# Kernel tuning notes

Measured on AMD Instinct MI355X. Metric: run time of the kernel, lower is better.

The kernel has to match this reference:

```python
import jax, jax.numpy as jnp
import numpy as np

I = 4  # input size
H = 4  # hidden size


def setup_inputs() -> dict:
    key = jax.random.key(0)
    ks = jax.random.split(key, 7)
    T, B = 2048, 8192
    s = 1.0 / np.sqrt(H)  # torch LSTM/Linear init scale
    x = jax.random.normal(ks[0], (T, B, I), dtype=jnp.float32)
    w_ih = jax.random.uniform(ks[1], (4 * H, I), minval=-s, maxval=s, dtype=jnp.float32)
    w_hh = jax.random.uniform(ks[2], (4 * H, H), minval=-s, maxval=s, dtype=jnp.float32)
    b_ih = jax.random.uniform(ks[3], (4 * H,), minval=-s, maxval=s, dtype=jnp.float32)
    b_hh = jax.random.uniform(ks[4], (4 * H,), minval=-s, maxval=s, dtype=jnp.float32)
    w_lin = jax.random.uniform(ks[5], (1, H), minval=-0.5, maxval=0.5, dtype=jnp.float32)
    b_lin = jax.random.uniform(ks[6], (1,), minval=-0.5, maxval=0.5, dtype=jnp.float32)
    return {"x": x, "w_ih": w_ih, "w_hh": w_hh, "b_ih": b_ih, "b_hh": b_hh,
            "w_lin": w_lin, "b_lin": b_lin}


def _lstm_scan(x, w_ih, w_hh, b_ih, b_hh):
    # x: (T, B, I). PyTorch gate order: i, f, g, o.
    T, B, _ = x.shape
    b = b_ih + b_hh  # (4H,)
    # Precompute input projections for all timesteps: (T, B, 4H)
    xg = jnp.einsum('tbi,gi->tbg', x, w_ih) + b

    def step(carry, xg_t):
        h, c = carry  # (B, H) each
        gates = xg_t + h @ w_hh.T  # (B, 4H)
        i, f, g, o = jnp.split(gates, 4, axis=-1)
        i = jax.nn.sigmoid(i)
        f = jax.nn.sigmoid(f)
        g = jnp.tanh(g)
        o = jax.nn.sigmoid(o)
        c = f * c + i * g
        h = o * jnp.tanh(c)
        return (h, c), h

    h0 = jnp.zeros((B, H), dtype=x.dtype)
    c0 = jnp.zeros((B, H), dtype=x.dtype)
    _, hs = jax.lax.scan(step, (h0, c0), xg)
    return hs  # (T, B, H)


def reference(x, w_ih, w_hh, b_ih, b_hh, w_lin, b_lin):
    hs = _lstm_scan(x, w_ih, w_hh, b_ih, b_hh)           # (T, B, H)
    out = jnp.einsum('tbh,oh->tbo', hs, w_lin) + b_lin   # (T, B, 1)
    return jax.nn.sigmoid(out)
```

## Files before the change

### kernel.cpp

```cpp
#include <hip/hip_runtime.h>

#define T_DIM 2048
#define B_DIM 8192
#define PH    256
#define SPH   8

__device__ __forceinline__ float dpp_qxor1(float v) {
  int i = __float_as_int(v);
  return __int_as_float(__builtin_amdgcn_update_dpp(i, i, 0xB1, 0xF, 0xF, false));
}
__device__ __forceinline__ float dpp_qxor2(float v) {
  int i = __float_as_int(v);
  return __int_as_float(__builtin_amdgcn_update_dpp(i, i, 0x4E, 0xF, 0xF, false));
}
__device__ __forceinline__ float dpp_qxor3(float v) {
  int i = __float_as_int(v);
  return __int_as_float(__builtin_amdgcn_update_dpp(i, i, 0x1B, 0xF, 0xF, false));
}
__device__ __forceinline__ float dpp_hmirror(float v) {
  int i = __float_as_int(v);
  return __int_as_float(__builtin_amdgcn_update_dpp(i, i, 0x141, 0xF, 0xF, false));
}

__global__ __launch_bounds__(768) void lstm_pc3_kernel(
    const float* __restrict__ x,
    const float* __restrict__ w_ih, const float* __restrict__ w_hh,
    const float* __restrict__ b_ih, const float* __restrict__ b_hh,
    const float* __restrict__ w_lin, const float* __restrict__ b_lin,
    float* __restrict__ out)
{
  __shared__ float xaBuf[2][4][64][17];
  __shared__ float hnBuf[2][4][64][9];

  const int tid  = threadIdx.x;
  const int wid  = tid >> 6;
  const int lane = tid & 63;
  const int pair = wid & 3;

  const float L2E = 1.4426950408889634f;
  const float cm2 = -2.0f * L2E;

  const int l = lane & 7;
  const int half1 = (l >> 2) & 1;
  const int e = (l & 3) ^ (half1 ? 3 : 0);
  const int grp = lane >> 3;
  const int rA = half1 * 4 + e;
  const int rB = 8 + half1 * 4 + e;
  const float sclA = -L2E;
  const float sclB = half1 ? -L2E : -2.0f * L2E;

  if (wid < 4) {
    __builtin_amdgcn_s_setprio(1);
    float whhA[4], whhB[4];
    #pragma unroll
    for (int k = 0; k < 4; ++k) {
      const int j = e ^ k;
      whhA[k] = sclA * w_hh[rA * 4 + j];
      whhB[k] = sclB * w_hh[rB * 4 + j];
    }
    const float sB = half1 ? 1.0f : 2.0f * cm2;
    const float oB = half1 ? 0.0f : -cm2;
    float ct = 0.0f, h0 = 0.0f, h1 = 0.0f, h2 = 0.0f, h3 = 0.0f;

    __syncthreads();

    for (int p = 0; p < PH; ++p) {
      const int d = p & 1;
      float xaA[SPH], xaB[SPH];
      #pragma unroll
      for (int k = 0; k < SPH; ++k) {
        xaA[k] = xaBuf[d][pair][lane][2 * k];
        xaB[k] = xaBuf[d][pair][lane][2 * k + 1];
      }
      #pragma unroll
      for (int k = 0; k < SPH; ++k) {
        float uA = fmaf(whhA[0], h0, xaA[k]);
        uA = fmaf(whhA[1], h1, uA);
        uA = fmaf(whhA[2], h2, uA);
        uA = fmaf(whhA[3], h3, uA);
        float uB = fmaf(whhB[0], h0, xaB[k]);
        uB = fmaf(whhB[1], h1, uB);
        uB = fmaf(whhB[2], h2, uB);
        uB = fmaf(whhB[3], h3, uB);
        const float aA = __builtin_amdgcn_rcpf(1.0f + __builtin_amdgcn_exp2f(uA));
        const float yB = __builtin_amdgcn_rcpf(1.0f + __builtin_amdgcn_exp2f(uB));
        const float aB = fmaf(sB, yB, oB);
        const float Z = half1 ? aA : aA * aB;
        const float W = dpp_hmirror(Z);
        const float F = half1 ? Z : W;
        const float P = half1 ? W : Z;
        ct = fmaf(F, ct, P);
        const float zc = __builtin_amdgcn_exp2f(ct);
        const float rc = __builtin_amdgcn_rcpf(1.0f + zc);
        const float Ox = dpp_hmirror(aB);
        const float ov = half1 ? aB : Ox;
        const float tc = fmaf(2.0f, rc, -1.0f);
        const float hn = ov * tc;
        h0 = hn;
        h1 = dpp_qxor1(hn);
        h2 = dpp_qxor2(hn);
        h3 = dpp_qxor3(hn);
        hnBuf[d][pair][lane][k] = hn;
      }
      __syncthreads();
    }
  } else if (wid < 8) {
    const int b = blockIdx.x * 32 + pair * 8 + grp;
    float wihA[4], wihB[4];
    #pragma unroll
    for (int k = 0; k < 4; ++k) {
      const int j = e ^ k;
      wihA[k] = sclA * w_ih[rA * 4 + j];
      wihB[k] = sclB * w_ih[rB * 4 + j];
    }
    const float biasA = sclA * (b_ih[rA] + b_hh[rA]);
    const float biasB = sclB * (b_ih[rB] + b_hh[rB]);

    const int XS = B_DIM * 4;
    const int xoff = b * 4 + e;

    float xc[SPH], xn[SPH];

    auto load8 = [&](float (&dst)[SPH], int ph) {
      const int base = xoff + ((ph & (PH - 1)) * SPH) * XS;
      #pragma unroll
      for (int k = 0; k < SPH; ++k) dst[k] = x[base + k * XS];
    };
    auto projWrite = [&](const float (&xr)[SPH], int dd) {
      #pragma unroll
      for (int k = 0; k < SPH; ++k) {
        const float xe = xr[k];
        const float x1 = dpp_qxor1(xe);
        const float x2 = dpp_qxor2(xe);
        const float x3 = dpp_qxor3(xe);
        float a = fmaf(wihA[0], xe, biasA);
        a = fmaf(wihA[1], x1, a);
        a = fmaf(wihA[2], x2, a);
        a = fmaf(wihA[3], x3, a);
        float bb = fmaf(wihB[0], xe, biasB);
        bb = fmaf(wihB[1], x1, bb);
        bb = fmaf(wihB[2], x2, bb);
        bb = fmaf(wihB[3], x3, bb);
        xaBuf[dd][pair][lane][2 * k]     = a;
        xaBuf[dd][pair][lane][2 * k + 1] = bb;
      }
    };

    load8(xc, 0);
    projWrite(xc, 0);
    load8(xn, 1);
    __syncthreads();

    for (int pp = 0; pp < PH; pp += 2) {
      projWrite(xn, 1);
      load8(xc, pp + 2);
      __syncthreads();
      projWrite(xc, 0);
      load8(xn, pp + 3);
      __syncthreads();
    }
  } else {
    const int og = lane & 7, oj = lane >> 3;
    const int ob = blockIdx.x * 32 + pair * 8 + og;
    float wl[4];
    #pragma unroll
    for (int j = 0; j < 4; ++j) wl[j] = -L2E * w_lin[j];
    const float blin = -L2E * b_lin[0];

    __syncthreads();

    for (int p = 0; p < PH; ++p) {
      __syncthreads();
      const int dh = p & 1;
      const float v0 = hnBuf[dh][pair][og * 8 + 0][oj];
      const float v1 = hnBuf[dh][pair][og * 8 + 1][oj];
      const float v2 = hnBuf[dh][pair][og * 8 + 2][oj];
      const float v3 = hnBuf[dh][pair][og * 8 + 3][oj];
      float m = fmaf(wl[0], v0, blin);
      m = fmaf(wl[1], v1, m);
      m = fmaf(wl[2], v2, m);
      m = fmaf(wl[3], v3, m);
      const float o = __builtin_amdgcn_rcpf(1.0f + __builtin_amdgcn_exp2f(m));
      out[(size_t)(p * SPH + oj) * B_DIM + ob] = o;
    }
  }
}

extern "C" void kernel_launch(void* const* d_in, const int* in_sizes, int n_in,
                              void* d_out, int out_size, void* d_ws, size_t ws_size,
                              hipStream_t stream) {
  const float* x     = (const float*)d_in[0];
  const float* w_ih  = (const float*)d_in[1];
  const float* w_hh  = (const float*)d_in[2];
  const float* b_ih  = (const float*)d_in[3];
  const float* b_hh  = (const float*)d_in[4];
  const float* w_lin = (const float*)d_in[5];
  const float* b_lin = (const float*)d_in[6];
  float* out = (float*)d_out;

  dim3 block(768);
  dim3 grid(B_DIM / 32);
  hipLaunchKernelGGL(lstm_pc3_kernel, grid, block, 0, stream,
                     x, w_ih, w_hh, b_ih, b_hh, w_lin, b_lin, out);
}
```

Before: 237.6 us.

## Replace block-wide barriers with per-pair LDS flag counters between producer/consumer warps

Swaps the workgroup-wide __syncthreads barriers for per-pair counters in shared memory. Each projection, recurrence and output-head wave publishes its progress with release stores and waits on its neighbours' counters with acquire loads and s_sleep. This lets the four independent batch groups drift apart instead of all 12 waves stalling on the slowest one. The projection buffer is also packed as float2, giving 64-bit LDS accesses. The cost is spin-polling overhead, and the ordering depends on the lgkmcnt wait plus workgroup-scope atomics being correct.

```diff
diff --git a/kernel.cpp b/kernel.cpp
--- a/kernel.cpp
+++ b/kernel.cpp
@@ -22,20 +22,38 @@
   return __int_as_float(__builtin_amdgcn_update_dpp(i, i, 0x141, 0xF, 0xF, false));
 }
 
-__global__ __launch_bounds__(768) void lstm_pc3_kernel(
+__global__ __launch_bounds__(768) void lstm_flag_kernel(
     const float* __restrict__ x,
     const float* __restrict__ w_ih, const float* __restrict__ w_hh,
     const float* __restrict__ b_ih, const float* __restrict__ b_hh,
     const float* __restrict__ w_lin, const float* __restrict__ b_lin,
     float* __restrict__ out)
 {
-  __shared__ float xaBuf[2][4][64][17];
-  __shared__ float hnBuf[2][4][64][9];
+  __shared__ float2 xaBuf[2][4][64][9];
+  __shared__ float  hnBuf[2][4][64][9];
+  __shared__ int    ctrs[12];
 
   const int tid  = threadIdx.x;
   const int wid  = tid >> 6;
   const int lane = tid & 63;
   const int pair = wid & 3;
+
+  if (tid < 12) ctrs[tid] = 0;
+  __syncthreads();
+
+  int* projC = &ctrs[pair];
+  int* recC  = &ctrs[4 + pair];
+  int* headC = &ctrs[8 + pair];
+
+  auto waitGE = [&](int* c, int v) {
+    while (__hip_atomic_load(c, __ATOMIC_ACQUIRE, __HIP_MEMORY_SCOPE_WORKGROUP) < v)
+      __builtin_amdgcn_s_sleep(1);
+  };
+  auto publish = [&](int* c, int v) {
+    asm volatile("s_waitcnt lgkmcnt(0)" ::: "memory");
+    if (lane == 0)
+      __hip_atomic_store(c, v, __ATOMIC_RELEASE, __HIP_MEMORY_SCOPE_WORKGROUP);
+  };
 
   const float L2E = 1.4426950408889634f;
   const float cm2 = -2.0f * L2E;
@@ -62,15 +80,16 @@
     const float oB = half1 ? 0.0f : -cm2;
     float ct = 0.0f, h0 = 0.0f, h1 = 0.0f, h2 = 0.0f, h3 = 0.0f;
 
-    __syncthreads();
-
     for (int p = 0; p < PH; ++p) {
+      waitGE(projC, p + 1);
+      waitGE(headC, p - 1);
       const int d = p & 1;
       float xaA[SPH], xaB[SPH];
       #pragma unroll
       for (int k = 0; k < SPH; ++k) {
-        xaA[k] = xaBuf[d][pair][lane][2 * k];
-        xaB[k] = xaBuf[d][pair][lane][2 * k + 1];
+        const float2 v = xaBuf[d][pair][lane][k];
+        xaA[k] = v.x;
+        xaB[k] = v.y;
       }
       #pragma unroll
       for (int k = 0; k < SPH; ++k) {
@@ -102,7 +121,7 @@
         h3 = dpp_qxor3(hn);
         hnBuf[d][pair][lane][k] = hn;
       }
-      __syncthreads();
+      publish(recC, p + 1);
     }
   } else if (wid < 8) {
     const int b = blockIdx.x * 32 + pair * 8 + grp;
@@ -141,23 +160,22 @@
         bb = fmaf(wihB[1], x1, bb);
         bb = fmaf(wihB[2], x2, bb);
         bb = fmaf(wihB[3], x3, bb);
-        xaBuf[dd][pair][lane][2 * k]     = a;
-        xaBuf[dd][pair][lane][2 * k + 1] = bb;
+        xaBuf[dd][pair][lane][k] = make_float2(a, bb);
       }
     };
 
     load8(xc, 0);
-    projWrite(xc, 0);
     load8(xn, 1);
-    __syncthreads();
-
-    for (int pp = 0; pp < PH; pp += 2) {
-      projWrite(xn, 1);
-      load8(xc, pp + 2);
-      __syncthreads();
-      projWrite(xc, 0);
-      load8(xn, pp + 3);
-      __syncthreads();
+    for (int p = 0; p < PH; ++p) {
+      waitGE(recC, p - 1);
+      if ((p & 1) == 0) {
+        projWrite(xc, 0);
+        load8(xc, p + 2);
+      } else {
+        projWrite(xn, 1);
+        load8(xn, p + 2);
+      }
+      publish(projC, p + 1);
     }
   } else {
     const int og = lane & 7, oj = lane >> 3;
@@ -167,11 +185,9 @@
     for (int j = 0; j < 4; ++j) wl[j] = -L2E * w_lin[j];
     const float blin = -L2E * b_lin[0];
 
-    __syncthreads();
-
-    for (int p = 0; p < PH; ++p) {
-      __syncthreads();
-      const int dh = p & 1;
+    for (int q = 0; q < PH; ++q) {
+      waitGE(recC, q + 1);
+      const int dh = q & 1;
       const float v0 = hnBuf[dh][pair][og * 8 + 0][oj];
       const float v1 = hnBuf[dh][pair][og * 8 + 1][oj];
       const float v2 = hnBuf[dh][pair][og * 8 + 2][oj];
@@ -181,7 +197,8 @@
       m = fmaf(wl[2], v2, m);
       m = fmaf(wl[3], v3, m);
       const float o = __builtin_amdgcn_rcpf(1.0f + __builtin_amdgcn_exp2f(m));
-      out[(size_t)(p * SPH + oj) * B_DIM + ob] = o;
+      out[(size_t)(q * SPH + oj) * B_DIM + ob] = o;
+      publish(headC, q + 1);
     }
   }
 }
@@ -200,6 +217,6 @@
 
   dim3 block(768);
   dim3 grid(B_DIM / 32);
-  hipLaunchKernelGGL(lstm_pc3_kernel, grid, block, 0, stream,
+  hipLaunchKernelGGL(lstm_flag_kernel, grid, block, 0, stream,
                      x, w_ih, w_hh, b_ih, b_hh, w_lin, b_lin, out);
 }
```

Result: slower. 247.6 us (+4.2%).
